# Kernel optimization log

Measured on AMD Instinct MI355X. Metric: run time of the kernel, lower is better.

Reference implementation:

```python
import jax, jax.numpy as jnp
import numpy as np

D_MODEL, D_STATE, EXPAND = 1024, 128, 2
E = D_MODEL * EXPAND          # 2048
N = D_STATE                   # 128
H = 1
P = E
TD = D_STATE // 2             # 64
Z_DIM = E + E + N + N + H + H + TD + H  # 4369
EPS = 1e-05
B_SZ, L = 4, 2048


def setup_inputs() -> dict:
    key = jax.random.key(0)
    ks = jax.random.split(key, 6)
    u = jax.random.normal(ks[0], (B_SZ, L, D_MODEL), dtype=jnp.float32)
    W_in = jax.random.normal(ks[1], (Z_DIM, D_MODEL), dtype=jnp.float32) * 0.02
    W_out = jax.random.normal(ks[2], (D_MODEL, E), dtype=jnp.float32) * 0.02
    w_normB = jnp.ones((N,), jnp.float32)
    w_normC = jnp.ones((N,), jnp.float32)
    B_bias = jnp.ones((N,), jnp.float32)
    C_bias = jnp.ones((N,), jnp.float32)
    # dt_bias buffer: dt_i ~ logU(0.001, 0.1); dt_bias = dt_i + log(-expm1(-dt_i))
    dt_i = jnp.exp(jax.random.uniform(ks[3], (H,)) * (np.log(0.1) - np.log(0.001)) + np.log(0.001))
    dt_i = jnp.clip(dt_i, 1e-4, None)
    dt_bias = dt_i + jnp.log(-jnp.expm1(-dt_i))
    A_log = jnp.full((H,), np.log(0.5), jnp.float32)
    return {"u": u, "W_in": W_in, "w_normB": w_normB, "w_normC": w_normC,
            "B_bias": B_bias, "C_bias": C_bias, "dt_bias": dt_bias,
            "A_log": A_log, "W_out": W_out}


def _rms(x, w):
    return x * jax.lax.rsqrt(jnp.mean(x * x, axis=-1, keepdims=True) + EPS) * w


def _rope(x, ang):
    half = x.shape[-1] // 2
    x1, x2 = x[..., :half], x[..., half:]
    c, s = jnp.cos(ang), jnp.sin(ang)
    return jnp.concatenate([x1 * c - x2 * s, x1 * s + x2 * c], axis=-1)


def reference(u, W_in, w_normB, w_normC, B_bias, C_bias, dt_bias, A_log, W_out):
    Bb, Ls, _ = u.shape
    z = u @ W_in.T  # [B, L, Z_DIM]
    o = 0
    def take(n):
        nonlocal o
        r = z[..., o:o + n]; o += n; return r
    x = jax.nn.silu(take(E))
    gate = jax.nn.silu(take(E))
    B_ = take(N)
    C_ = take(N)
    dt_ = take(H)
    A_ = take(H)
    th = take(TD)
    lam_ = take(H)

    dt = jax.nn.softplus(dt_ + dt_bias)          # [B, L, H]
    A = -jax.nn.softplus(A_ + A_log)             # [B, L, H]
    lam = jax.nn.sigmoid(lam_)                   # [B, L, H]
    alpha = jnp.exp(dt * A)                      # [B, L, H]

    B_ = _rms(B_, w_normB) + B_bias
    C_ = _rms(C_, w_normC) + C_bias
    ca = jnp.cumsum(jnp.mean(dt, axis=-1, keepdims=True) * th, axis=1)  # [B, L, TD]
    B_ = _rope(B_, ca)
    C_ = _rope(C_, ca)

    xh = x.reshape(Bb, Ls, H, P)
    xp = jnp.concatenate([jnp.zeros_like(xh[:, :1]), xh[:, :-1]], axis=1)  # roll + zero t=0
    lh = lam[..., None]
    xt = lh * xh + (1.0 - lh) * alpha[..., None] * xp  # [B, L, H, P]

    # fallback SSM: per-channel mean drive, per-head scalar A (mean over batch+time)
    u_mean = jnp.mean(xt, axis=-1)               # [B, L, H]
    A_bar = jnp.mean(A, axis=(0, 1))             # [H]
    dA = jnp.exp(dt * A_bar)                     # [B, L, H]
    dBu = dt[..., None] * B_[:, :, None, :] * u_mean[..., None]  # [B, L, H, N]

    def step(state, xs):
        dA_t, dBu_t, C_t = xs                    # [B,H], [B,H,N], [B,N]
        state = dA_t[..., None] * state + dBu_t  # [B, H, N]
        y_t = jnp.einsum('bhn,bn->bh', state, C_t)
        return state, y_t

    state0 = jnp.zeros((Bb, H, N), dtype=xt.dtype)
    _, ys = jax.lax.scan(step, state0,
                         (jnp.moveaxis(dA, 1, 0), jnp.moveaxis(dBu, 1, 0), jnp.moveaxis(C_, 1, 0)))
    outs = jnp.moveaxis(ys, 0, 1)                # [B, L, H]
    y = jnp.broadcast_to(outs, (Bb, Ls, E))      # H=1 expanded to E
    return (y * gate) @ W_out.T
```

## Files before the change

kernel.cpp:

```cpp
#include <hip/hip_runtime.h>
#include <cstdint>
#include <cstddef>

typedef __bf16 bf16_t;
typedef bf16_t bf16x8 __attribute__((ext_vector_type(8)));
typedef bf16_t bf16x4 __attribute__((ext_vector_type(4)));
typedef float f32x4 __attribute__((ext_vector_type(4)));

#define B_SZ    4
#define LSEQ    2048
#define DMODEL  1024
#define EDIM    2048
#define ZDIM    4419
#define ZPAD    4608
#define ROWS    (B_SZ*LSEQ)
#define EPSV    1e-5f

#define LDU     1088
#define LDG     2112

#define SCHUNK  128
#define SCLEN   (LSEQ/SCHUNK)
#define RCH     128
#define RCLEN   (LSEQ/RCH)

__device__ __forceinline__ float softplus_f(float x){
  return fmaxf(x, 0.f) + log1pf(expf(-fabsf(x)));
}
__device__ __forceinline__ float sigmoid_f(float x){ return 1.f/(1.f+expf(-x)); }
__device__ __forceinline__ float silu_f(float x){ return x/(1.f+expf(-x)); }

__device__ __forceinline__ void gload_lds16(const void* g, void* l){
  __builtin_amdgcn_global_load_lds(
      (const __attribute__((address_space(1))) void*)g,
      (__attribute__((address_space(3))) void*)l, 16, 0, 0);
}

__device__ __forceinline__ float blockReduce128(float v, float* red, int t){
  red[t] = v; __syncthreads();
  #pragma unroll
  for (int off = 64; off > 0; off >>= 1){
    if (t < off) red[t] += red[t+off];
    __syncthreads();
  }
  float r = red[0];
  __syncthreads();
  return r;
}

__global__ __launch_bounds__(256) void prep_kernel(
    const float4* __restrict__ u4, const float4* __restrict__ win4,
    const float4* __restrict__ wout4,
    bf16_t* __restrict__ ubf, bf16_t* __restrict__ winbf, bf16_t* __restrict__ woutbf,
    float* __restrict__ Asum, float* __restrict__ xraw)
{
  size_t i = (size_t)blockIdx.x*256 + threadIdx.x;
  if (i == 0) Asum[0] = 0.f;
  if (i < ROWS) xraw[i] = 0.f;
  const size_t NU4 = (size_t)ROWS*DMODEL/4;
  const size_t NW4 = (size_t)ZPAD*DMODEL/4;
  const size_t NO4 = (size_t)DMODEL*EDIM/4;
  if (i < NU4){
    float4 v = u4[i];
    size_t e = i*4, row = e>>10, col = e&1023;
    bf16x4 o = { (bf16_t)v.x, (bf16_t)v.y, (bf16_t)v.z, (bf16_t)v.w };
    *(bf16x4*)&ubf[row*LDU + col] = o;
    return;
  }
  i -= NU4;
  if (i < NW4){
    size_t e = i*4, row = e>>10, col = e&1023;
    bf16x4 o;
    if (row < (size_t)ZDIM){
      float4 v = win4[i];
      o = bf16x4{ (bf16_t)v.x, (bf16_t)v.y, (bf16_t)v.z, (bf16_t)v.w };
    } else {
      o = bf16x4{ (bf16_t)0.f, (bf16_t)0.f, (bf16_t)0.f, (bf16_t)0.f };
    }
    *(bf16x4*)&winbf[row*LDU + col] = o;
    return;
  }
  i -= NW4;
  if (i < NO4){
    float4 v = wout4[i];
    size_t e = i*4, row = e>>11, col = e&2047;
    bf16x4 o = { (bf16_t)v.x, (bf16_t)v.y, (bf16_t)v.z, (bf16_t)v.w };
    *(bf16x4*)&woutbf[row*LDG + col] = o;
  }
}

template<int LDA_, int LDW_, int NT, int NXT, int MODE>
__global__ __launch_bounds__(256) void gemmM_kernel(
    const bf16_t* __restrict__ A0, const bf16_t* __restrict__ W0,
    float* __restrict__ xraw, bf16_t* __restrict__ o_g, float* __restrict__ o_z,
    const float* __restrict__ scale, float* __restrict__ o_f)
{
  __shared__ __align__(16) bf16_t lds[8192];

  const int tid = threadIdx.x;
  const int wid = tid>>6, lane = tid&63;
  const int wr = wid>>1, wc = wid&1;
  const int lr = lane&15, hi = lane>>4;

  constexpr int NWG = (MODE==0) ? NXT*(ROWS/128) : NXT*(ROWS/128)*2;
  const int id = blockIdx.x;
  const int rid = (id & 7)*(NWG/8) + (id>>3);
  int bx, by, kz = 0;
  if (MODE == 0){ bx = rid % NXT; by = rid / NXT; }
  else { kz = rid / (NXT*(ROWS/128)); int r2 = rid % (NXT*(ROWS/128));
         bx = r2 % NXT; by = r2 / NXT; }
  const int m0 = by*128, n0 = bx*128;
  const size_t kzo = (size_t)kz*1024;

  f32x4 acc[4][4] = {};

  const bf16_t* pA[2]; const bf16_t* pW[2];
  int dstA[2], dstB[2];
  #pragma unroll
  for (int q = 0; q < 2; ++q){
    int cidx = q*256 + tid;
    int row = cidx>>2, dch = cidx&3;
    int gs = (dch - (row>>1)) & 3;
    pA[q] = A0 + kzo + (size_t)(m0+row)*LDA_ + gs*8;
    pW[q] = W0 + kzo + (size_t)(n0+row)*LDW_ + gs*8;
    dstA[q] = cidx*8;
    dstB[q] = 4096 + cidx*8;
  }

  int aoff[4], boff[4];
  {
    int R0 = wr*64 + lr;
    int cA = (hi + (R0>>1)) & 3;
    #pragma unroll
    for (int m = 0; m < 4; ++m) aoff[m] = (R0 + 16*m)*32 + cA*8;
    int R0b = wc*64 + lr;
    int cB = (hi + (R0b>>1)) & 3;
    #pragma unroll
    for (int n = 0; n < 4; ++n) boff[n] = 4096 + (R0b + 16*n)*32 + cB*8;
  }

  #pragma unroll 1
  for (int t = 0; t < NT; ++t){
    gload_lds16(pA[0], &lds[dstA[0]]);
    gload_lds16(pA[1], &lds[dstA[1]]);
    gload_lds16(pW[0], &lds[dstB[0]]);
    gload_lds16(pW[1], &lds[dstB[1]]);
    pA[0] += 32; pA[1] += 32; pW[0] += 32; pW[1] += 32;
    __syncthreads();
    bf16x8 bfr[4];
    #pragma unroll
    for (int n = 0; n < 4; ++n) bfr[n] = *(const bf16x8*)&lds[boff[n]];
    #pragma unroll
    for (int m = 0; m < 4; ++m){
      bf16x8 af = *(const bf16x8*)&lds[aoff[m]];
      #pragma unroll
      for (int n = 0; n < 4; ++n)
        acc[m][n] = __builtin_amdgcn_mfma_f32_16x16x32_bf16(af, bfr[n], acc[m][n], 0,0,0);
    }
    __syncthreads();
  }

  if (MODE == 0 && n0 < 2048){
    #pragma unroll
    for (int m = 0; m < 4; ++m){
      #pragma unroll
      for (int i = 0; i < 4; ++i){
        float p = 0.f;
        #pragma unroll
        for (int n = 0; n < 4; ++n) p += silu_f(acc[m][n][i]);
        p += __shfl_xor(p, 8); p += __shfl_xor(p, 4);
        p += __shfl_xor(p, 2); p += __shfl_xor(p, 1);
        if (lr == 0){
          int r = m0 + wr*64 + m*16 + (hi<<2) + i;
          atomicAdd(xraw + r, p);
        }
      }
    }
  } else if (MODE == 0){
    #pragma unroll
    for (int m = 0; m < 4; ++m){
      int rowb = m0 + wr*64 + m*16 + (hi<<2);
      #pragma unroll
      for (int n = 0; n < 4; ++n){
        int col = n0 + wc*64 + n*16 + lr;
        #pragma unroll
        for (int i = 0; i < 4; ++i){
          int r = rowb + i;
          float v = acc[m][n][i];
          if (col < 4096)      o_g[(size_t)r*LDG + (col-2048)] = (bf16_t)silu_f(v);
          else if (col < 4480) o_z[(size_t)r*384 + (col-4096)] = v;
        }
      }
    }
  } else {
    #pragma unroll
    for (int m = 0; m < 4; ++m){
      int rowb = m0 + wr*64 + m*16 + (hi<<2);
      #pragma unroll
      for (int i = 0; i < 4; ++i){
        int r = rowb + i;
        float s = scale[r];
        #pragma unroll
        for (int n = 0; n < 4; ++n){
          int col = n0 + wc*64 + n*16 + lr;
          atomicAdd(o_f + (size_t)r*DMODEL + col, acc[m][n][i]*s);
        }
      }
    }
  }
}

__global__ __launch_bounds__(128) void fuse_kernel(
    const float* __restrict__ xraw, const float* __restrict__ zs,
    const float* __restrict__ wnB, const float* __restrict__ wnC,
    const float* __restrict__ Bb, const float* __restrict__ Cb,
    const float* __restrict__ dtb, const float* __restrict__ Alog,
    float* __restrict__ Bn, float* __restrict__ Cn, float* __restrict__ dtth,
    float* __restrict__ dts, float* __restrict__ alphas, float* __restrict__ lams,
    float* __restrict__ xbar, float* Asum)
{
  __shared__ float red[128];
  int r = blockIdx.x, t = threadIdx.x;
  const float* zr = zs + (size_t)r*384;
  float bv = zr[t], cv = zr[128+t];
  float b2 = blockReduce128(bv*bv, red, t);
  float c2 = blockReduce128(cv*cv, red, t);
  float rb = rsqrtf(b2*(1.f/128.f) + EPSV);
  float rc = rsqrtf(c2*(1.f/128.f) + EPSV);
  Bn[(size_t)r*128 + t] = bv*rb*wnB[t] + Bb[t];
  Cn[(size_t)r*128 + t] = cv*rc*wnC[t] + Cb[t];

  float dt = softplus_f(zr[256] + dtb[0]);
  if (t < 64) dtth[(size_t)r*64 + t] = dt * zr[258+t];
  if (t == 0){
    float Av  = -softplus_f(zr[257] + Alog[0]);
    float lam = sigmoid_f(zr[322]);
    dts[r]    = dt;
    alphas[r] = expf(dt*Av);
    lams[r]   = lam;
    xbar[r]   = xraw[r] * (1.f/2048.f);
    atomicAdd(Asum, Av);
  }
}

__global__ __launch_bounds__(64) void rope_sum_kernel(
    const float* __restrict__ dtth, float* __restrict__ csum)
{
  int b  = blockIdx.x >> 7;
  int ch = blockIdx.x & 127;
  int d  = threadIdx.x;
  const float* base = dtth + ((size_t)b*LSEQ + (size_t)ch*RCLEN)*64 + d;
  float s = 0.f;
  #pragma unroll
  for (int i = 0; i < RCLEN; ++i) s += base[(size_t)i*64];
  csum[((size_t)b*RCH + ch)*64 + d] = s;
}

__global__ __launch_bounds__(64) void rope_prefix_kernel(float* __restrict__ csum)
{
  int b = blockIdx.x, d = threadIdx.x;
  float s = 0.f;
  for (int c = 0; c < RCH; ++c){
    size_t idx = ((size_t)b*RCH + c)*64 + d;
    float v = csum[idx]; csum[idx] = s; s += v;
  }
}

__global__ __launch_bounds__(64) void rope_apply_kernel(
    const float* __restrict__ dtth, const float* __restrict__ csum,
    float* __restrict__ Bn, float* __restrict__ Cn)
{
  int b  = blockIdx.x >> 7;
  int ch = blockIdx.x & 127;
  int d  = threadIdx.x;
  float ca = csum[((size_t)b*RCH + ch)*64 + d];
  int l0 = ch*RCLEN;
  const float* base = dtth + ((size_t)b*LSEQ)*64 + d;
  for (int l = l0; l < l0 + RCLEN; ++l){
    ca += base[(size_t)l*64];
    float sn, cs;
    sincosf(ca, &sn, &cs);
    size_t ro = ((size_t)b*LSEQ + l)*128;
    float b1 = Bn[ro+d], b2v = Bn[ro+64+d];
    Bn[ro+d]    = b1*cs - b2v*sn;
    Bn[ro+64+d] = b1*sn + b2v*cs;
    float c1 = Cn[ro+d], c2v = Cn[ro+64+d];
    Cn[ro+d]    = c1*cs - c2v*sn;
    Cn[ro+64+d] = c1*sn + c2v*cs;
  }
}

__global__ __launch_bounds__(64) void scan_local_kernel(
    const float* __restrict__ dts, const float* __restrict__ alphas,
    const float* __restrict__ lams, const float* __restrict__ xbar,
    const float* __restrict__ Asum,
    const float* __restrict__ Bn, const float* __restrict__ Cn,
    float* __restrict__ ylocal, float* __restrict__ Pfix,
    float* __restrict__ Sfin, float* __restrict__ Dch)
{
  int b  = blockIdx.x / SCHUNK;
  int ch = blockIdx.x % SCHUNK;
  int n  = threadIdx.x;
  float Abar = Asum[0] * (1.f/(float)ROWS);
  float s1 = 0.f, s2 = 0.f, P = 1.f;
  int l0 = ch*SCLEN;
  #pragma unroll
  for (int i = 0; i < SCLEN; ++i){
    int l = l0 + i;
    size_t r = (size_t)b*LSEQ + l;
    float dt = dts[r], lam = lams[r], al = alphas[r], xb = xbar[r];
    float xp = (l > 0) ? xbar[r-1] : 0.f;
    float um = lam*xb + (1.f-lam)*al*xp;
    float dA = expf(dt*Abar);
    float coef = dt*um;
    size_t ro = r*128;
    s1 = dA*s1 + coef*Bn[ro+n];
    s2 = dA*s2 + coef*Bn[ro+64+n];
    P *= dA;
    float p = s1*Cn[ro+n] + s2*Cn[ro+64+n];
    #pragma unroll
    for (int off = 32; off > 0; off >>= 1) p += __shfl_down(p, off);
    if (n == 0){ ylocal[r] = p; Pfix[r] = P; }
  }
  size_t so = ((size_t)b*SCHUNK + ch)*128;
  Sfin[so + n]      = s1;
  Sfin[so + 64 + n] = s2;
  if (n == 0) Dch[b*SCHUNK + ch] = P;
}

__global__ __launch_bounds__(128) void scan_carry_kernel(
    const float* __restrict__ Sfin, const float* __restrict__ Dch,
    float* __restrict__ Sin)
{
  int b = blockIdx.x;
  int n = threadIdx.x;
  float s = 0.f;
  for (int c = 0; c < SCHUNK; ++c){
    size_t so = ((size_t)b*SCHUNK + c)*128;
    Sin[so + n] = s;
    s = Dch[b*SCHUNK + c]*s + Sfin[so + n];
  }
}

__global__ __launch_bounds__(256) void scan_fix_kernel(
    const float* __restrict__ Cn, const float* __restrict__ Sin,
    const float* __restrict__ ylocal, const float* __restrict__ Pfix,
    float* __restrict__ outsv)
{
  int r = blockIdx.x*4 + (threadIdx.x>>6);
  int n = threadIdx.x & 63;
  int b  = r / LSEQ;
  int ch = (r % LSEQ) / SCLEN;
  const float* si = Sin + ((size_t)b*SCHUNK + ch)*128;
  size_t ro = (size_t)r*128;
  float p = Cn[ro+n]*si[n] + Cn[ro+64+n]*si[64+n];
  #pragma unroll
  for (int off = 32; off > 0; off >>= 1) p += __shfl_down(p, off);
  if (n == 0) outsv[r] = ylocal[r] + Pfix[r]*p;
}

extern "C" void kernel_launch(void* const* d_in, const int* in_sizes, int n_in,
                              void* d_out, int out_size, void* d_ws, size_t ws_size,
                              hipStream_t stream)
{
  const float* u    = (const float*)d_in[0];
  const float* W_in = (const float*)d_in[1];
  const float* wnB  = (const float*)d_in[2];
  const float* wnC  = (const float*)d_in[3];
  const float* Bb   = (const float*)d_in[4];
  const float* Cb   = (const float*)d_in[5];
  const float* dtb  = (const float*)d_in[6];
  const float* Alog = (const float*)d_in[7];
  const float* Wout = (const float*)d_in[8];
  float* out = (float*)d_out;
  char* ws = (char*)d_ws;

  constexpr size_t OFF_ASUM = 0;
  constexpr size_t OFF_UBF  = 256;
  constexpr size_t SZ_UBF   = (size_t)ROWS*LDU*2;
  constexpr size_t OFF_WIN  = OFF_UBF + SZ_UBF;
  constexpr size_t SZ_WIN   = (size_t)ZPAD*LDU*2;
  constexpr size_t OFF_WOUT = OFF_WIN + SZ_WIN;
  constexpr size_t SZ_WOUT  = (size_t)DMODEL*LDG*2;
  constexpr size_t OFF_G    = OFF_WOUT + SZ_WOUT;
  constexpr size_t SZ_G     = (size_t)ROWS*LDG*2;
  constexpr size_t OFF_ZS   = OFF_G + SZ_G;
  constexpr size_t SZ_ZS    = (size_t)ROWS*384*4;
  constexpr size_t OFF_BN   = OFF_ZS + SZ_ZS;
  constexpr size_t SZ_BN    = (size_t)ROWS*128*4;
  constexpr size_t OFF_CN   = OFF_BN + SZ_BN;
  constexpr size_t OFF_DTTH = OFF_CN + SZ_BN;
  constexpr size_t SZ_DTTH  = (size_t)ROWS*64*4;
  constexpr size_t OFF_XRAW = OFF_DTTH + SZ_DTTH;
  constexpr size_t OFF_DT   = OFF_XRAW + (size_t)ROWS*4;
  constexpr size_t OFF_AL   = OFF_DT  + (size_t)ROWS*4;
  constexpr size_t OFF_LAM  = OFF_AL  + (size_t)ROWS*4;
  constexpr size_t OFF_XB   = OFF_LAM + (size_t)ROWS*4;
  constexpr size_t OFF_OUTS = OFF_XB  + (size_t)ROWS*4;
  constexpr size_t OFF_YLOC = OFF_OUTS + (size_t)ROWS*4;
  constexpr size_t OFF_PFIX = OFF_YLOC + (size_t)ROWS*4;
  constexpr size_t OFF_SFIN = OFF_PFIX + (size_t)ROWS*4;
  constexpr size_t SZ_SFIN  = (size_t)B_SZ*SCHUNK*128*4;
  constexpr size_t OFF_DCH  = OFF_SFIN + SZ_SFIN;
  constexpr size_t OFF_SIN  = OFF_DCH + (size_t)B_SZ*SCHUNK*4;
  constexpr size_t OFF_CSUM = OFF_SIN + SZ_SFIN;

  float*  Asum   = (float*) (ws + OFF_ASUM);
  bf16_t* ubf    = (bf16_t*)(ws + OFF_UBF);
  bf16_t* winbf  = (bf16_t*)(ws + OFF_WIN);
  bf16_t* woutbf = (bf16_t*)(ws + OFF_WOUT);
  bf16_t* gbuf   = (bf16_t*)(ws + OFF_G);
  float*  zsb    = (float*) (ws + OFF_ZS);
  float*  Bn     = (float*) (ws + OFF_BN);
  float*  Cn     = (float*) (ws + OFF_CN);
  float*  dtth   = (float*) (ws + OFF_DTTH);
  float*  xraw   = (float*) (ws + OFF_XRAW);
  float*  dts    = (float*) (ws + OFF_DT);
  float*  alphas = (float*) (ws + OFF_AL);
  float*  lams   = (float*) (ws + OFF_LAM);
  float*  xbar   = (float*) (ws + OFF_XB);
  float*  outsv  = (float*) (ws + OFF_OUTS);
  float*  ylocal = (float*) (ws + OFF_YLOC);
  float*  Pfix   = (float*) (ws + OFF_PFIX);
  float*  Sfin   = (float*) (ws + OFF_SFIN);
  float*  Dch    = (float*) (ws + OFF_DCH);
  float*  Sin    = (float*) (ws + OFF_SIN);
  float*  csum   = (float*) (ws + OFF_CSUM);

  {
    size_t total4 = ((size_t)ROWS*DMODEL + (size_t)ZPAD*DMODEL + (size_t)DMODEL*EDIM)/4;
    int blocks = (int)((total4 + 255)/256);
    prep_kernel<<<blocks, 256, 0, stream>>>(
        (const float4*)u, (const float4*)W_in, (const float4*)Wout,
        ubf, winbf, woutbf, Asum, xraw);
  }
  hipMemsetAsync(out, 0, (size_t)ROWS*DMODEL*sizeof(float), stream);

  gemmM_kernel<LDU, LDU, 32, ZPAD/128, 0>
      <<<(ZPAD/128)*(ROWS/128), 256, 0, stream>>>(
      ubf, winbf, xraw, gbuf, zsb, nullptr, nullptr);
  fuse_kernel<<<ROWS, 128, 0, stream>>>(xraw, zsb, wnB, wnC, Bb, Cb, dtb, Alog,
                                        Bn, Cn, dtth, dts, alphas, lams, xbar, Asum);
  rope_sum_kernel<<<B_SZ*RCH, 64, 0, stream>>>(dtth, csum);
  rope_prefix_kernel<<<B_SZ, 64, 0, stream>>>(csum);
  rope_apply_kernel<<<B_SZ*RCH, 64, 0, stream>>>(dtth, csum, Bn, Cn);
  scan_local_kernel<<<B_SZ*SCHUNK, 64, 0, stream>>>(dts, alphas, lams, xbar, Asum,
                                                    Bn, Cn, ylocal, Pfix, Sfin, Dch);
  scan_carry_kernel<<<B_SZ, 128, 0, stream>>>(Sfin, Dch, Sin);
  scan_fix_kernel<<<ROWS/4, 256, 0, stream>>>(Cn, Sin, ylocal, Pfix, outsv);
  gemmM_kernel<LDG, LDG, 32, DMODEL/128, 1>
      <<<2*(DMODEL/128)*(ROWS/128), 256, 0, stream>>>(
      gbuf, woutbf, nullptr, nullptr, nullptr, outsv, out);
}
```

Measured before the change: 389.8 us.

## Pre-shuffle weights into MFMA fragment layout and double-buffer GEMM with 128x256 tiles

The prep kernel now writes W_in and W_out in a fragment-major layout so each lane can load its B operand directly from global memory into registers, skipping LDS. The GEMM tiles grow to 128x256 with 8 N-fragments per wave, and the A tile is double-buffered in LDS with register prefetch of B, replacing two barriers per k-step with one. The aim is to halve LDS traffic and barrier stalls and to overlap loads with MFMA work. The cost is more accumulator registers and fewer workgroups, which may lower occupancy, and the B loads now rely on the cache.

```diff
diff --git a/kernel.cpp b/kernel.cpp
--- a/kernel.cpp
+++ b/kernel.cpp
@@ -51,7 +51,7 @@
 __global__ __launch_bounds__(256) void prep_kernel(
     const float4* __restrict__ u4, const float4* __restrict__ win4,
     const float4* __restrict__ wout4,
-    bf16_t* __restrict__ ubf, bf16_t* __restrict__ winbf, bf16_t* __restrict__ woutbf,
+    bf16_t* __restrict__ ubf, bf16_t* __restrict__ winSh, bf16_t* __restrict__ woutSh,
     float* __restrict__ Asum, float* __restrict__ xraw)
 {
   size_t i = (size_t)blockIdx.x*256 + threadIdx.x;
@@ -69,7 +69,7 @@
   }
   i -= NU4;
   if (i < NW4){
-    size_t e = i*4, row = e>>10, col = e&1023;
+    size_t e = i*4, row = e>>10, k = e&1023;
     bf16x4 o;
     if (row < (size_t)ZDIM){
       float4 v = win4[i];
@@ -77,21 +77,27 @@
     } else {
       o = bf16x4{ (bf16_t)0.f, (bf16_t)0.f, (bf16_t)0.f, (bf16_t)0.f };
     }
-    *(bf16x4*)&winbf[row*LDU + col] = o;
+    int ntile = (int)(row>>4), colf = (int)(row&15);
+    int kt = (int)(k>>5), koct = (int)((k>>3)&3), ko = (int)(k&7);
+    size_t off = (((size_t)ntile*32 + kt)<<9) + (koct<<7) + (colf<<3) + ko;
+    *(bf16x4*)&winSh[off] = o;
     return;
   }
   i -= NW4;
   if (i < NO4){
     float4 v = wout4[i];
-    size_t e = i*4, row = e>>11, col = e&2047;
+    size_t e = i*4, row = e>>11, k = e&2047;
     bf16x4 o = { (bf16_t)v.x, (bf16_t)v.y, (bf16_t)v.z, (bf16_t)v.w };
-    *(bf16x4*)&woutbf[row*LDG + col] = o;
-  }
-}
-
-template<int LDA_, int LDW_, int NT, int NXT, int MODE>
-__global__ __launch_bounds__(256) void gemmM_kernel(
-    const bf16_t* __restrict__ A0, const bf16_t* __restrict__ W0,
+    int ntile = (int)(row>>4), colf = (int)(row&15);
+    int kt = (int)(k>>5), koct = (int)((k>>3)&3), ko = (int)(k&7);
+    size_t off = (((size_t)ntile*64 + kt)<<9) + (koct<<7) + (colf<<3) + ko;
+    *(bf16x4*)&woutSh[off] = o;
+  }
+}
+
+template<int LDA_, int NKT, int NT, int NXT, int MODE>
+__global__ __launch_bounds__(256, 2) void gemmV_kernel(
+    const bf16_t* __restrict__ A0, const bf16_t* __restrict__ Bsh,
     float* __restrict__ xraw, bf16_t* __restrict__ o_g, float* __restrict__ o_z,
     const float* __restrict__ scale, float* __restrict__ o_f)
 {
@@ -102,62 +108,88 @@
   const int wr = wid>>1, wc = wid&1;
   const int lr = lane&15, hi = lane>>4;
 
-  constexpr int NWG = (MODE==0) ? NXT*(ROWS/128) : NXT*(ROWS/128)*2;
+  constexpr int MB = ROWS/128;
+  constexpr int NWG = (MODE==0) ? NXT*MB : NXT*MB*2;
   const int id = blockIdx.x;
   const int rid = (id & 7)*(NWG/8) + (id>>3);
   int bx, by, kz = 0;
   if (MODE == 0){ bx = rid % NXT; by = rid / NXT; }
-  else { kz = rid / (NXT*(ROWS/128)); int r2 = rid % (NXT*(ROWS/128));
-         bx = r2 % NXT; by = r2 / NXT; }
-  const int m0 = by*128, n0 = bx*128;
-  const size_t kzo = (size_t)kz*1024;
-
-  f32x4 acc[4][4] = {};
-
-  const bf16_t* pA[2]; const bf16_t* pW[2];
-  int dstA[2], dstB[2];
-  #pragma unroll
-  for (int q = 0; q < 2; ++q){
-    int cidx = q*256 + tid;
-    int row = cidx>>2, dch = cidx&3;
-    int gs = (dch - (row>>1)) & 3;
-    pA[q] = A0 + kzo + (size_t)(m0+row)*LDA_ + gs*8;
-    pW[q] = W0 + kzo + (size_t)(n0+row)*LDW_ + gs*8;
-    dstA[q] = cidx*8;
-    dstB[q] = 4096 + cidx*8;
-  }
-
-  int aoff[4], boff[4];
+  else { kz = rid / (NXT*MB); int r2 = rid % (NXT*MB); bx = r2 % NXT; by = r2 / NXT; }
+  const int m0 = by*128, n0 = bx*256;
+  const int kt0 = kz*32;
+
+  f32x4 acc[4][8] = {};
+
+  const bf16_t* pA0; const bf16_t* pA1;
+  int dA0, dA1;
+  {
+    int c0 = tid,      r0 = c0>>2, d0 = c0&3, g0 = (d0 - (r0>>1)) & 3;
+    int c1 = 256+tid,  r1 = c1>>2, d1 = c1&3, g1 = (d1 - (r1>>1)) & 3;
+    pA0 = A0 + (size_t)kz*1024 + (size_t)(m0+r0)*LDA_ + g0*8;
+    pA1 = A0 + (size_t)kz*1024 + (size_t)(m0+r1)*LDA_ + g1*8;
+    dA0 = c0*8; dA1 = c1*8;
+  }
+  int aoff[4];
   {
     int R0 = wr*64 + lr;
     int cA = (hi + (R0>>1)) & 3;
     #pragma unroll
     for (int m = 0; m < 4; ++m) aoff[m] = (R0 + 16*m)*32 + cA*8;
-    int R0b = wc*64 + lr;
-    int cB = (hi + (R0b>>1)) & 3;
-    #pragma unroll
-    for (int n = 0; n < 4; ++n) boff[n] = 4096 + (R0b + 16*n)*32 + cB*8;
-  }
+  }
+  const bf16_t* bB0 = Bsh + (((size_t)((n0>>4) + wc*8)*NKT + kt0)<<9) + lane*8;
+  int koff = 0;
+
+  bf16x8 bA[8], bB[8], af[4];
+
+  gload_lds16(pA0, &lds[dA0]); pA0 += 32;
+  gload_lds16(pA1, &lds[dA1]); pA1 += 32;
+  #pragma unroll
+  for (int n = 0; n < 8; ++n)
+    bA[n] = *(const bf16x8*)(bB0 + (size_t)n*(NKT*512) + koff);
+  koff += 512;
+  asm volatile("s_waitcnt vmcnt(8)" ::: "memory");
+  __builtin_amdgcn_s_barrier();
 
   #pragma unroll 1
-  for (int t = 0; t < NT; ++t){
-    gload_lds16(pA[0], &lds[dstA[0]]);
-    gload_lds16(pA[1], &lds[dstA[1]]);
-    gload_lds16(pW[0], &lds[dstB[0]]);
-    gload_lds16(pW[1], &lds[dstB[1]]);
-    pA[0] += 32; pA[1] += 32; pW[0] += 32; pW[1] += 32;
-    __syncthreads();
-    bf16x8 bfr[4];
-    #pragma unroll
-    for (int n = 0; n < 4; ++n) bfr[n] = *(const bf16x8*)&lds[boff[n]];
-    #pragma unroll
-    for (int m = 0; m < 4; ++m){
-      bf16x8 af = *(const bf16x8*)&lds[aoff[m]];
-      #pragma unroll
-      for (int n = 0; n < 4; ++n)
-        acc[m][n] = __builtin_amdgcn_mfma_f32_16x16x32_bf16(af, bfr[n], acc[m][n], 0,0,0);
-    }
-    __syncthreads();
+  for (int t2 = 0; t2 < NT/2; ++t2){
+    {
+      #pragma unroll
+      for (int m = 0; m < 4; ++m) af[m] = *(const bf16x8*)&lds[aoff[m]];
+      gload_lds16(pA0, &lds[4096 + dA0]); pA0 += 32;
+      gload_lds16(pA1, &lds[4096 + dA1]); pA1 += 32;
+      #pragma unroll
+      for (int n = 0; n < 8; ++n)
+        bB[n] = *(const bf16x8*)(bB0 + (size_t)n*(NKT*512) + koff);
+      koff += 512;
+      #pragma unroll
+      for (int m = 0; m < 4; ++m)
+        #pragma unroll
+        for (int n = 0; n < 8; ++n)
+          acc[m][n] = __builtin_amdgcn_mfma_f32_16x16x32_bf16(af[m], bA[n], acc[m][n], 0,0,0);
+      asm volatile("s_waitcnt vmcnt(8)" ::: "memory");
+      __builtin_amdgcn_s_barrier();
+    }
+    {
+      #pragma unroll
+      for (int m = 0; m < 4; ++m) af[m] = *(const bf16x8*)&lds[4096 + aoff[m]];
+      const bool pf = (t2 < NT/2 - 1);
+      if (pf){
+        gload_lds16(pA0, &lds[dA0]); pA0 += 32;
+        gload_lds16(pA1, &lds[dA1]); pA1 += 32;
+        #pragma unroll
+        for (int n = 0; n < 8; ++n)
+          bA[n] = *(const bf16x8*)(bB0 + (size_t)n*(NKT*512) + koff);
+        koff += 512;
+      }
+      #pragma unroll
+      for (int m = 0; m < 4; ++m)
+        #pragma unroll
+        for (int n = 0; n < 8; ++n)
+          acc[m][n] = __builtin_amdgcn_mfma_f32_16x16x32_bf16(af[m], bB[n], acc[m][n], 0,0,0);
+      if (pf) { asm volatile("s_waitcnt vmcnt(8)" ::: "memory"); }
+      else    { asm volatile("s_waitcnt vmcnt(0)" ::: "memory"); }
+      __builtin_amdgcn_s_barrier();
+    }
   }
 
   if (MODE == 0 && n0 < 2048){
@@ -167,7 +199,7 @@
       for (int i = 0; i < 4; ++i){
         float p = 0.f;
         #pragma unroll
-        for (int n = 0; n < 4; ++n) p += silu_f(acc[m][n][i]);
+        for (int n = 0; n < 8; ++n) p += silu_f(acc[m][n][i]);
         p += __shfl_xor(p, 8); p += __shfl_xor(p, 4);
         p += __shfl_xor(p, 2); p += __shfl_xor(p, 1);
         if (lr == 0){
@@ -181,8 +213,8 @@
     for (int m = 0; m < 4; ++m){
       int rowb = m0 + wr*64 + m*16 + (hi<<2);
       #pragma unroll
-      for (int n = 0; n < 4; ++n){
-        int col = n0 + wc*64 + n*16 + lr;
+      for (int n = 0; n < 8; ++n){
+        int col = n0 + wc*128 + n*16 + lr;
         #pragma unroll
         for (int i = 0; i < 4; ++i){
           int r = rowb + i;
@@ -201,8 +233,8 @@
         int r = rowb + i;
         float s = scale[r];
         #pragma unroll
-        for (int n = 0; n < 4; ++n){
-          int col = n0 + wc*64 + n*16 + lr;
+        for (int n = 0; n < 8; ++n){
+          int col = n0 + wc*128 + n*16 + lr;
           atomicAdd(o_f + (size_t)r*DMODEL + col, acc[m][n][i]*s);
         }
       }
@@ -407,8 +439,8 @@
 
   float*  Asum   = (float*) (ws + OFF_ASUM);
   bf16_t* ubf    = (bf16_t*)(ws + OFF_UBF);
-  bf16_t* winbf  = (bf16_t*)(ws + OFF_WIN);
-  bf16_t* woutbf = (bf16_t*)(ws + OFF_WOUT);
+  bf16_t* winSh  = (bf16_t*)(ws + OFF_WIN);
+  bf16_t* woutSh = (bf16_t*)(ws + OFF_WOUT);
   bf16_t* gbuf   = (bf16_t*)(ws + OFF_G);
   float*  zsb    = (float*) (ws + OFF_ZS);
   float*  Bn     = (float*) (ws + OFF_BN);
@@ -432,13 +464,13 @@
     int blocks = (int)((total4 + 255)/256);
     prep_kernel<<<blocks, 256, 0, stream>>>(
         (const float4*)u, (const float4*)W_in, (const float4*)Wout,
-        ubf, winbf, woutbf, Asum, xraw);
+        ubf, winSh, woutSh, Asum, xraw);
   }
   hipMemsetAsync(out, 0, (size_t)ROWS*DMODEL*sizeof(float), stream);
 
-  gemmM_kernel<LDU, LDU, 32, ZPAD/128, 0>
-      <<<(ZPAD/128)*(ROWS/128), 256, 0, stream>>>(
-      ubf, winbf, xraw, gbuf, zsb, nullptr, nullptr);
+  gemmV_kernel<LDU, 32, 32, ZPAD/256, 0>
+      <<<(ZPAD/256)*(ROWS/128), 256, 0, stream>>>(
+      ubf, winSh, xraw, gbuf, zsb, nullptr, nullptr);
   fuse_kernel<<<ROWS, 128, 0, stream>>>(xraw, zsb, wnB, wnC, Bb, Cb, dtb, Alog,
                                         Bn, Cn, dtth, dts, alphas, lams, xbar, Asum);
   rope_sum_kernel<<<B_SZ*RCH, 64, 0, stream>>>(dtth, csum);
@@ -448,7 +480,7 @@
                                                     Bn, Cn, ylocal, Pfix, Sfin, Dch);
   scan_carry_kernel<<<B_SZ, 128, 0, stream>>>(Sfin, Dch, Sin);
   scan_fix_kernel<<<ROWS/4, 256, 0, stream>>>(Cn, Sin, ylocal, Pfix, outsv);
-  gemmM_kernel<LDG, LDG, 32, DMODEL/128, 1>
-      <<<2*(DMODEL/128)*(ROWS/128), 256, 0, stream>>>(
-      gbuf, woutbf, nullptr, nullptr, nullptr, outsv, out);
-}
+  gemmV_kernel<LDG, 64, 32, DMODEL/256, 1>
+      <<<2*(DMODEL/256)*(ROWS/128), 256, 0, stream>>>(
+      gbuf, woutSh, nullptr, nullptr, nullptr, outsv, out);
+}
```

After: 382.0 us. 2.0% less time.
